# Performance work log

Measured on AMD Instinct MI355X. Metric: run time of the kernel, lower is better.

Reference implementation:

```python
import jax, jax.numpy as jnp
import numpy as np
from jax import lax

EPS = 1e-5
TRUNK_C, REG_C, GPOOL_C = 256, 192, 64
B, H, W = 256, 19, 19


def setup_inputs() -> dict:
    key = jax.random.key(0)
    ks = jax.random.split(key, 18)
    def bn_params(k, c):
        k1, k2, k3, k4 = jax.random.split(k, 4)
        return (jax.random.normal(k1, (c,)) * 0.1 + 1.0,   # gamma
                jax.random.normal(k2, (c,)) * 0.1,          # beta
                jax.random.normal(k3, (c,)) * 0.1,          # running mean
                jax.random.uniform(k4, (c,)) * 0.5 + 0.5)   # running var
    bn1_g, bn1_b, bn1_m, bn1_v = bn_params(ks[0], TRUNK_C)
    bn1b_g, bn1b_b, bn1b_m, bn1b_v = bn_params(ks[1], GPOOL_C)
    bn2_g, bn2_b, bn2_m, bn2_v = bn_params(ks[2], REG_C)
    x = jax.random.normal(ks[3], (B, TRUNK_C, H, W), dtype=jnp.float32)
    w1a = jax.random.normal(ks[4], (REG_C, TRUNK_C, 3, 3), dtype=jnp.float32) * (1.0 / np.sqrt(TRUNK_C * 9))
    w1b = jax.random.normal(ks[5], (GPOOL_C, TRUNK_C, 3, 3), dtype=jnp.float32) * (1.0 / np.sqrt(TRUNK_C * 9))
    w_lin = jax.random.normal(ks[6], (REG_C, 3 * GPOOL_C), dtype=jnp.float32) * (1.0 / np.sqrt(3 * GPOOL_C))
    w2 = jax.random.normal(ks[7], (TRUNK_C, REG_C, 3, 3), dtype=jnp.float32) * (1.0 / np.sqrt(REG_C * 9))
    return {
        'x': x, 'bn1_g': bn1_g, 'bn1_b': bn1_b, 'bn1_m': bn1_m, 'bn1_v': bn1_v,
        'w1a': w1a, 'w1b': w1b,
        'bn1b_g': bn1b_g, 'bn1b_b': bn1b_b, 'bn1b_m': bn1b_m, 'bn1b_v': bn1b_v,
        'w_lin': w_lin,
        'bn2_g': bn2_g, 'bn2_b': bn2_b, 'bn2_m': bn2_m, 'bn2_v': bn2_v,
        'w2': w2,
    }


def _bn(x, g, b, m, v):
    # inference batchnorm over channel dim of NCHW
    inv = g / jnp.sqrt(v + EPS)
    return (x - m[:, None, None]) * inv[:, None, None] + b[:, None, None]


def _mish(x):
    return x * jnp.tanh(jax.nn.softplus(x))


def _conv(x, w):
    return lax.conv_general_dilated(x, w, (1, 1), 'SAME',
                                    dimension_numbers=('NCHW', 'OIHW', 'NCHW'))


def _kata_gpool(x):
    # x: [B, C, H, W] -> [B, 3C]: mean, mean*(sqrt(N)-14)/10, max
    b, c, h, w = x.shape
    n = float(h * w)
    sqrt_n = n ** 0.5
    mean = jnp.sum(x, axis=(2, 3)) / n
    max_val = jnp.max(x, axis=(2, 3))
    scaled_mean = mean * ((sqrt_n - 14.0) / 10.0)
    return jnp.concatenate([mean, scaled_mean, max_val], axis=1)


def reference(x, bn1_g, bn1_b, bn1_m, bn1_v, w1a, w1b,
              bn1b_g, bn1b_b, bn1b_m, bn1b_v, w_lin,
              bn2_g, bn2_b, bn2_m, bn2_v, w2):
    out = _mish(_bn(x, bn1_g, bn1_b, bn1_m, bn1_v))
    reg = _conv(out, w1a)                       # [B, REG_C, H, W]
    gp = _conv(out, w1b)                        # [B, GPOOL_C, H, W]
    gp = _mish(_bn(gp, bn1b_g, bn1b_b, bn1b_m, bn1b_v))
    gp_pooled = _kata_gpool(gp)                 # [B, 3*GPOOL_C]
    gp_out = gp_pooled @ w_lin.T                # [B, REG_C]
    reg = reg + gp_out[:, :, None, None]
    out2 = _mish(_bn(reg, bn2_g, bn2_b, bn2_m, bn2_v))
    out2 = _conv(out2, w2)
    return out2 + x
```

## Files before the change

### kernel.cpp

```cpp
#include <hip/hip_runtime.h>
#include <hip/hip_bf16.h>
#include <math.h>


#define BATCH   256
#define TRUNK_C 256
#define REG_C   192
#define GPOOL_C 64
#define HH      19
#define WW      19
#define HW      361
#define PP      441
#define EPS     1e-5f

typedef __hip_bfloat16 bf16;
typedef __attribute__((ext_vector_type(8))) short short8;
typedef __attribute__((ext_vector_type(4))) float floatx4;

__device__ __forceinline__ float b2f(bf16 v) { return __bfloat162float(v); }
__device__ __forceinline__ bf16  f2b(float v) { return __float2bfloat16(v); }

__device__ __forceinline__ float mish_f(float v) {
    if (v > 20.0f) return v;
    float u = __expf(v);
    float n = u * (u + 2.0f);
    return v * __fdividef(n, n + 2.0f);
}

__device__ __forceinline__ void gload_lds16(const void* gsrc, void* lds) {
    __builtin_amdgcn_global_load_lds(
        (const __attribute__((address_space(1))) void*)gsrc,
        (__attribute__((address_space(3))) void*)lds, 16, 0, 0);
}

__global__ void prep_kernel(
    const float* g1, const float* b1, const float* m1, const float* v1,
    const float* g1b, const float* b1b, const float* m1b, const float* v1b,
    const float* g2, const float* b2, const float* m2, const float* v2,
    const float* __restrict__ w1a, const float* __restrict__ w1b,
    const float* __restrict__ w2,
    bf16* __restrict__ w1c_p, bf16* __restrict__ w2_p,
    bf16* __restrict__ act_pad, bf16* __restrict__ reg_pad,
    float* bnbuf)
{
    const int T1  = 16 * 72 * 64 * 8;
    const int T2  = 16 * 54 * 64 * 8;
    const int TW  = T1 + T2;
    const int TBa = BATCH * 80 * 32;
    const int TBr = BATCH * 80 * 24;
    int i = blockIdx.x * blockDim.x + threadIdx.x;
    if (i < TW) {
        if (i < T1) {
            int j = i & 7, lane = (i >> 3) & 63;
            int kc = (i >> 9) % 72, cog = (i >> 9) / 72;
            int co = cog * 16 + (lane & 15);
            int k = kc * 32 + ((lane >> 4) << 3) + j;
            int r = k >> 8, ci = k & 255;
            float v = (co < 192) ? w1a[co * 2304 + ci * 9 + r]
                                 : w1b[(co - 192) * 2304 + ci * 9 + r];
            w1c_p[i] = f2b(v);
        } else {
            int i2 = i - T1;
            int j = i2 & 7, lane = (i2 >> 3) & 63;
            int kc = (i2 >> 9) % 54, cog = (i2 >> 9) / 54;
            int co = cog * 16 + (lane & 15);
            int k = kc * 32 + ((lane >> 4) << 3) + j;
            int r = k / 192, ci = k % 192;
            w2_p[i2] = f2b(w2[co * 1728 + ci * 9 + r]);
        }
    } else if (i < TW + TBa + TBr) {
        int j = i - TW;
        bool isact = j < TBa;
        if (!isact) j -= TBa;
        int nb = isact ? 32 : 24;
        int b = j / (80 * nb);
        int rem = j - b * (80 * nb);
        int e = rem / nb, g = rem - (rem / nb) * nb;
        int pp;
        if (e < 21) pp = e;
        else if (e < 42) pp = 420 + (e - 21);
        else if (e < 61) pp = (e - 41) * 21;
        else pp = (e - 60) * 21 + 20;
        short8 z = {0, 0, 0, 0, 0, 0, 0, 0};
        if (isact) *(short8*)(act_pad + ((size_t)b * PP + pp) * TRUNK_C + g * 8) = z;
        else       *(short8*)(reg_pad + ((size_t)b * PP + pp) * REG_C + g * 8) = z;
    } else {
        int t = i - (TW + TBa + TBr);
        if (t < 256) {
            float s = g1[t] / sqrtf(v1[t] + EPS);
            bnbuf[t] = s;
            bnbuf[256 + t] = b1[t] - m1[t] * s;
        } else if (t < 320) {
            int c = t - 256;
            float s = g1b[c] / sqrtf(v1b[c] + EPS);
            bnbuf[512 + c] = s;
            bnbuf[576 + c] = b1b[c] - m1b[c] * s;
        } else if (t < 512) {
            int c = t - 320;
            float s = g2[c] / sqrtf(v2[c] + EPS);
            bnbuf[640 + c] = s;
            bnbuf[832 + c] = b2[c] - m2[c] * s;
        }
    }
}

__global__ __launch_bounds__(256)
void bn1_mish_t_kernel(const float* __restrict__ x, const float* __restrict__ bnbuf,
                       bf16* __restrict__ act_pad) {
    __shared__ float lds[256][32];
    int pc = blockIdx.x;
    int b  = blockIdx.y;
    int t  = threadIdx.x;
    int p0 = pc * 32;
    int px = t & 31;
#pragma unroll
    for (int it = 0; it < 32; ++it) {
        int ci = it * 8 + (t >> 5);
        int p  = p0 + px;
        float v = 0.0f;
        if (p < HW) v = x[((size_t)b * TRUNK_C + ci) * HW + p];
        v = v * bnbuf[ci] + bnbuf[256 + ci];
        lds[ci][px ^ (ci >> 3)] = mish_f(v);
    }
    __syncthreads();
#pragma unroll
    for (int it = 0; it < 4; ++it) {
        int pl = it * 8 + (t >> 5);
        int p  = p0 + pl;
        if (p >= HW) continue;
        int ch = t & 31;
        short8 vv;
#pragma unroll
        for (int j = 0; j < 8; ++j) {
            bf16 h = f2b(lds[ch * 8 + j][pl ^ ch]);
            short s;
            __builtin_memcpy(&s, &h, 2);
            vv[j] = s;
        }
        int pp = (p / WW + 1) * 21 + (p % WW + 1);
        *(short8*)(act_pad + ((size_t)b * PP + pp) * TRUNK_C + ch * 8) = vv;
    }
}

__global__ __launch_bounds__(256, 3)
void conv1_kernel(const bf16* __restrict__ act,
                  const bf16* __restrict__ wfrag,
                  bf16* __restrict__ reg_out,
                  bf16* __restrict__ gp_out,
                  const float* __restrict__ ep_scale, const float* __restrict__ ep_bias) {
    const int CIN = 256, NKC = 72;
    __shared__ __align__(16) bf16 atile[4][128 * 32];
    const int b   = blockIdx.x;
    const int mt  = blockIdx.y;
    const int nh  = blockIdx.z;
    const int t   = threadIdx.x;
    const int w   = t >> 6, lane = t & 63;
    const int mi  = w >> 1, ni = w & 1;
    const int l15 = lane & 15, quad = lane >> 4;

    int row0 = t >> 2;
    int sq   = t & 3;
    int ss   = sq ^ ((row0 >> 1) & 3);
    int sp0  = mt * 128 + row0;      if (sp0 > 360) sp0 = 360;
    int sp1  = mt * 128 + row0 + 64; if (sp1 > 360) sp1 = 360;
    const bf16* sb0 = act + ((size_t)b * PP + (sp0 / WW) * 21 + (sp0 % WW)) * CIN + (ss << 3);
    const bf16* sb1 = act + ((size_t)b * PP + (sp1 / WW) * 21 + (sp1 % WW)) * CIN + (ss << 3);

    const bf16* wb[4];
#pragma unroll
    for (int ns = 0; ns < 4; ++ns)
        wb[ns] = wfrag + ((size_t)(nh * 8 + ni * 4 + ns) * NKC * 64 + lane) * 8;

    int aoff[4];
#pragma unroll
    for (int ms = 0; ms < 4; ++ms) {
        int row = mi * 64 + ms * 16 + l15;
        aoff[ms] = row * 32 + ((quad ^ ((row >> 1) & 3)) << 3);
    }

    auto stage = [&](int buf, int kc) {
        int r = kc >> 3, c = kc & 7;
        int off = ((r / 3) * 21 + (r % 3)) * CIN + (c << 5);
        bf16* dst = &atile[buf][w << 9];
        gload_lds16(sb0 + off, dst);
        gload_lds16(sb1 + off, dst + 2048);
    };

    floatx4 acc[4][4];
#pragma unroll
    for (int i = 0; i < 4; ++i)
#pragma unroll
        for (int j = 0; j < 4; ++j) acc[i][j] = (floatx4){0.f, 0.f, 0.f, 0.f};

    short8 afr[4], bfrA[4], bfrB[4];
    stage(0, 0);
    stage(1, 1);
    asm volatile("" ::: "memory");
#pragma unroll
    for (int ns = 0; ns < 4; ++ns) bfrA[ns] = *(const short8*)(wb[ns]);
    asm volatile("" ::: "memory");
    stage(2, 2);

    for (int kc = 0; kc < NKC; kc += 2) {
        if (kc == 0) asm volatile("s_waitcnt vmcnt(8)" ::: "memory");
        else         asm volatile("s_waitcnt vmcnt(12)" ::: "memory");
        __builtin_amdgcn_sched_barrier(0);
        __builtin_amdgcn_s_barrier();
        __builtin_amdgcn_sched_barrier(0);
#pragma unroll
        for (int ns = 0; ns < 4; ++ns)
            bfrB[ns] = *(const short8*)(wb[ns] + (size_t)(kc + 1) * 512);
        asm volatile("" ::: "memory");
        {
            int s = kc + 3; if (s > NKC - 1) s = NKC - 1;
            stage((kc + 3) & 3, s);
        }
        {
            const bf16* at = atile[kc & 3];
#pragma unroll
            for (int ms = 0; ms < 4; ++ms)
                afr[ms] = *(const short8*)(at + aoff[ms]);
        }
#pragma unroll
        for (int ms = 0; ms < 4; ++ms)
#pragma unroll
            for (int ns = 0; ns < 4; ++ns)
                acc[ms][ns] = __builtin_amdgcn_mfma_f32_16x16x32_bf16(
                    afr[ms], bfrA[ns], acc[ms][ns], 0, 0, 0);

        asm volatile("s_waitcnt vmcnt(12)" ::: "memory");
        __builtin_amdgcn_sched_barrier(0);
        __builtin_amdgcn_s_barrier();
        __builtin_amdgcn_sched_barrier(0);
        {
            int nb = kc + 2; if (nb > NKC - 1) nb = NKC - 1;
#pragma unroll
            for (int ns = 0; ns < 4; ++ns)
                bfrA[ns] = *(const short8*)(wb[ns] + (size_t)nb * 512);
        }
        asm volatile("" ::: "memory");
        {
            int s = kc + 4; if (s > NKC - 1) s = NKC - 1;
            stage((kc + 4) & 3, s);
        }
        {
            const bf16* at = atile[(kc + 1) & 3];
#pragma unroll
            for (int ms = 0; ms < 4; ++ms)
                afr[ms] = *(const short8*)(at + aoff[ms]);
        }
#pragma unroll
        for (int ms = 0; ms < 4; ++ms)
#pragma unroll
            for (int ns = 0; ns < 4; ++ns)
                acc[ms][ns] = __builtin_amdgcn_mfma_f32_16x16x32_bf16(
                    afr[ms], bfrB[ns], acc[ms][ns], 0, 0, 0);
    }

    float scl[4], bia[4];
#pragma unroll
    for (int ns = 0; ns < 4; ++ns) {
        int co = (nh * 8 + ni * 4 + ns) * 16 + l15;
        if (co >= 192) { scl[ns] = ep_scale[co - 192]; bia[ns] = ep_bias[co - 192]; }
    }
#pragma unroll
    for (int ms = 0; ms < 4; ++ms) {
#pragma unroll
        for (int rg = 0; rg < 4; ++rg) {
            int p = mt * 128 + mi * 64 + ms * 16 + quad * 4 + rg;
            if (p > 360) continue;
            size_t ppad = (size_t)b * PP + (p / WW + 1) * 21 + (p % WW + 1);
#pragma unroll
            for (int ns = 0; ns < 4; ++ns) {
                int co = (nh * 8 + ni * 4 + ns) * 16 + l15;
                float v = acc[ms][ns][rg];
                if (co < 192) {
                    reg_out[ppad * REG_C + co] = f2b(v);
                } else {
                    v = mish_f(v * scl[ns] + bia[ns]);
                    gp_out[((size_t)b * HW + p) * GPOOL_C + (co - 192)] = f2b(v);
                }
            }
        }
    }
}

__global__ __launch_bounds__(256, 3)
void conv2_kernel(const bf16* __restrict__ act,
                  const bf16* __restrict__ wfrag,
                  const float* __restrict__ resid,
                  float* __restrict__ out) {
    const int CIN = 192, NKC = 54;
    __shared__ __align__(16) bf16 atile[4][128 * 32];
    const int b   = blockIdx.x;
    const int mt  = blockIdx.y;
    const int nh  = blockIdx.z;
    const int t   = threadIdx.x;
    const int w   = t >> 6, lane = t & 63;
    const int pw  = w >> 1, cw = w & 1;
    const int l15 = lane & 15, quad = lane >> 4;

    int row0 = t >> 2;
    int sq   = t & 3;
    int ss   = sq ^ ((row0 >> 1) & 3);
    int sp0  = mt * 128 + row0;      if (sp0 > 360) sp0 = 360;
    int sp1  = mt * 128 + row0 + 64; if (sp1 > 360) sp1 = 360;
    const bf16* sb0 = act + ((size_t)b * PP + (sp0 / WW) * 21 + (sp0 % WW)) * CIN + (ss << 3);
    const bf16* sb1 = act + ((size_t)b * PP + (sp1 / WW) * 21 + (sp1 % WW)) * CIN + (ss << 3);

    const bf16* wb[4];
#pragma unroll
    for (int ms = 0; ms < 4; ++ms)
        wb[ms] = wfrag + ((size_t)(nh * 8 + cw * 4 + ms) * NKC * 64 + lane) * 8;

    int aoff[4];
#pragma unroll
    for (int ns = 0; ns < 4; ++ns) {
        int row = pw * 64 + ns * 16 + l15;
        aoff[ns] = row * 32 + ((quad ^ ((row >> 1) & 3)) << 3);
    }

    auto stage = [&](int buf, int kc) {
        int r = kc / 6, c = kc % 6;
        int off = ((r / 3) * 21 + (r % 3)) * CIN + (c << 5);
        bf16* dst = &atile[buf][w << 9];
        gload_lds16(sb0 + off, dst);
        gload_lds16(sb1 + off, dst + 2048);
    };

    floatx4 acc[4][4];
#pragma unroll
    for (int i = 0; i < 4; ++i)
#pragma unroll
        for (int j = 0; j < 4; ++j) acc[i][j] = (floatx4){0.f, 0.f, 0.f, 0.f};

    short8 bfa[4], wfrA[4], wfrB[4];
    stage(0, 0);
    stage(1, 1);
    asm volatile("" ::: "memory");
#pragma unroll
    for (int ms = 0; ms < 4; ++ms) wfrA[ms] = *(const short8*)(wb[ms]);
    asm volatile("" ::: "memory");
    stage(2, 2);

    for (int kc = 0; kc < NKC; kc += 2) {
        if (kc == 0) asm volatile("s_waitcnt vmcnt(8)" ::: "memory");
        else         asm volatile("s_waitcnt vmcnt(12)" ::: "memory");
        __builtin_amdgcn_sched_barrier(0);
        __builtin_amdgcn_s_barrier();
        __builtin_amdgcn_sched_barrier(0);
#pragma unroll
        for (int ms = 0; ms < 4; ++ms)
            wfrB[ms] = *(const short8*)(wb[ms] + (size_t)(kc + 1) * 512);
        asm volatile("" ::: "memory");
        {
            int s = kc + 3; if (s > NKC - 1) s = NKC - 1;
            stage((kc + 3) & 3, s);
        }
        {
            const bf16* at = atile[kc & 3];
#pragma unroll
            for (int ns = 0; ns < 4; ++ns)
                bfa[ns] = *(const short8*)(at + aoff[ns]);
        }
#pragma unroll
        for (int ms = 0; ms < 4; ++ms)
#pragma unroll
            for (int ns = 0; ns < 4; ++ns)
                acc[ms][ns] = __builtin_amdgcn_mfma_f32_16x16x32_bf16(
                    wfrA[ms], bfa[ns], acc[ms][ns], 0, 0, 0);

        asm volatile("s_waitcnt vmcnt(12)" ::: "memory");
        __builtin_amdgcn_sched_barrier(0);
        __builtin_amdgcn_s_barrier();
        __builtin_amdgcn_sched_barrier(0);
        {
            int nb = kc + 2; if (nb > NKC - 1) nb = NKC - 1;
#pragma unroll
            for (int ms = 0; ms < 4; ++ms)
                wfrA[ms] = *(const short8*)(wb[ms] + (size_t)nb * 512);
        }
        asm volatile("" ::: "memory");
        {
            int s = kc + 4; if (s > NKC - 1) s = NKC - 1;
            stage((kc + 4) & 3, s);
        }
        {
            const bf16* at = atile[(kc + 1) & 3];
#pragma unroll
            for (int ns = 0; ns < 4; ++ns)
                bfa[ns] = *(const short8*)(at + aoff[ns]);
        }
#pragma unroll
        for (int ms = 0; ms < 4; ++ms)
#pragma unroll
            for (int ns = 0; ns < 4; ++ns)
                acc[ms][ns] = __builtin_amdgcn_mfma_f32_16x16x32_bf16(
                    wfrB[ms], bfa[ns], acc[ms][ns], 0, 0, 0);
    }

#pragma unroll
    for (int ns = 0; ns < 4; ++ns) {
        int p = mt * 128 + pw * 64 + ns * 16 + l15;
        if (p > 360) continue;
#pragma unroll
        for (int ms = 0; ms < 4; ++ms) {
#pragma unroll
            for (int rg = 0; rg < 4; ++rg) {
                int co = (nh * 8 + cw * 4 + ms) * 16 + quad * 4 + rg;
                size_t idx = ((size_t)b * TRUNK_C + co) * HW + p;
                out[idx] = acc[ms][ns][rg] + resid[idx];
            }
        }
    }
}

__global__ void gpool_lin_kernel(const bf16* __restrict__ gp, const float* __restrict__ w_lin,
                                 float* __restrict__ gpout) {
    __shared__ float ls[4][64], lm[4][64];
    __shared__ float pooled_s[192];
    int b = blockIdx.x;
    int t = threadIdx.x;
    int c = t & 63, sub = t >> 6;
    float s = 0.0f, mx = -1e30f;
    for (int p = sub; p < HW; p += 4) {
        float v = b2f(gp[((size_t)b * HW + p) * GPOOL_C + c]);
        s += v;
        mx = fmaxf(mx, v);
    }
    ls[sub][c] = s; lm[sub][c] = mx;
    __syncthreads();
    if (t < 64) {
        float ss = ls[0][t] + ls[1][t] + ls[2][t] + ls[3][t];
        float mm = fmaxf(fmaxf(lm[0][t], lm[1][t]), fmaxf(lm[2][t], lm[3][t]));
        float mean = ss * (1.0f / 361.0f);
        pooled_s[t] = mean;
        pooled_s[64 + t] = mean * 0.5f;
        pooled_s[128 + t] = mm;
    }
    __syncthreads();
    if (t < 192) {
        const float4* wr4 = (const float4*)(w_lin + t * 192);
        float acc = 0.0f;
#pragma unroll 8
        for (int j = 0; j < 48; ++j) {
            float4 wv = wr4[j];
            acc = fmaf(pooled_s[j * 4 + 0], wv.x, acc);
            acc = fmaf(pooled_s[j * 4 + 1], wv.y, acc);
            acc = fmaf(pooled_s[j * 4 + 2], wv.z, acc);
            acc = fmaf(pooled_s[j * 4 + 3], wv.w, acc);
        }
        gpout[b * 192 + t] = acc;
    }
}

__global__ __launch_bounds__(256)
void add_bn2_mish_kernel(bf16* __restrict__ reg_pad, const float* __restrict__ gpout,
                         const float* __restrict__ bnbuf) {
    const int total = BATCH * HW * 24;
    int i = blockIdx.x * blockDim.x + threadIdx.x;
    if (i >= total) return;
    int g  = i % 24;
    int bp = i / 24;
    int p  = bp % HW;
    int b  = bp / HW;
    int pp = (p / WW + 1) * 21 + (p % WW + 1);
    size_t idx = ((size_t)b * PP + pp) * REG_C + g * 8;
    short8 v = *(const short8*)(reg_pad + idx);
    const float* gpo = gpout + b * 192 + g * 8;
    const float* sc  = bnbuf + 640 + g * 8;
    const float* bi  = bnbuf + 832 + g * 8;
    short8 o;
#pragma unroll
    for (int j = 0; j < 8; ++j) {
        short sj = v[j];
        bf16 h;
        __builtin_memcpy(&h, &sj, 2);
        float f = b2f(h) + gpo[j];
        f = f * sc[j] + bi[j];
        h = f2b(mish_f(f));
        __builtin_memcpy(&sj, &h, 2);
        o[j] = sj;
    }
    *(short8*)(reg_pad + idx) = o;
}

extern "C" void kernel_launch(void* const* d_in, const int* in_sizes, int n_in,
                              void* d_out, int out_size, void* d_ws, size_t ws_size,
                              hipStream_t stream) {
    const float* x     = (const float*)d_in[0];
    const float* bn1_g = (const float*)d_in[1];
    const float* bn1_b = (const float*)d_in[2];
    const float* bn1_m = (const float*)d_in[3];
    const float* bn1_v = (const float*)d_in[4];
    const float* w1a   = (const float*)d_in[5];
    const float* w1b   = (const float*)d_in[6];
    const float* bn1b_g = (const float*)d_in[7];
    const float* bn1b_b = (const float*)d_in[8];
    const float* bn1b_m = (const float*)d_in[9];
    const float* bn1b_v = (const float*)d_in[10];
    const float* w_lin  = (const float*)d_in[11];
    const float* bn2_g  = (const float*)d_in[12];
    const float* bn2_b  = (const float*)d_in[13];
    const float* bn2_m  = (const float*)d_in[14];
    const float* bn2_v  = (const float*)d_in[15];
    const float* w2     = (const float*)d_in[16];
    float* out = (float*)d_out;

    char* ws = (char*)d_ws;
    size_t off = 0;
    auto alloc = [&](size_t bytes) {
        void* p = ws + off;
        off += (bytes + 255) & ~(size_t)255;
        return p;
    };
    bf16*  act_pad = (bf16*)alloc((size_t)BATCH * PP * TRUNK_C * sizeof(bf16));
    bf16*  reg_pad = (bf16*)alloc((size_t)BATCH * PP * REG_C * sizeof(bf16));
    bf16*  gp      = (bf16*)alloc((size_t)BATCH * HW * GPOOL_C * sizeof(bf16));
    bf16*  w1c_p   = (bf16*)alloc((size_t)16 * 72 * 64 * 8 * sizeof(bf16));
    bf16*  w2_p    = (bf16*)alloc((size_t)16 * 54 * 64 * 8 * sizeof(bf16));
    float* gpout   = (float*)alloc((size_t)BATCH * 192 * sizeof(float));
    float* bnbuf   = (float*)alloc(1024 * sizeof(float));
    (void)ws_size;

    {
        const int total = (16 * 72 * 64 * 8) + (16 * 54 * 64 * 8)
                        + BATCH * 80 * 32 + BATCH * 80 * 24 + 512;
        hipLaunchKernelGGL(prep_kernel, dim3((total + 255) / 256), dim3(256), 0, stream,
                           bn1_g, bn1_b, bn1_m, bn1_v,
                           bn1b_g, bn1b_b, bn1b_m, bn1b_v,
                           bn2_g, bn2_b, bn2_m, bn2_v,
                           w1a, w1b, w2, w1c_p, w2_p, act_pad, reg_pad, bnbuf);
    }

    hipLaunchKernelGGL(bn1_mish_t_kernel, dim3(12, BATCH), dim3(256), 0, stream,
                       x, bnbuf, act_pad);

    hipLaunchKernelGGL(conv1_kernel, dim3(BATCH, 3, 2), dim3(256), 0, stream,
                       act_pad, w1c_p, reg_pad, gp, bnbuf + 512, bnbuf + 576);

    hipLaunchKernelGGL(gpool_lin_kernel, dim3(BATCH), dim3(256), 0, stream,
                       gp, w_lin, gpout);

    {
        int total = BATCH * HW * 24;
        hipLaunchKernelGGL(add_bn2_mish_kernel, dim3((total + 255) / 256), dim3(256), 0, stream,
                           reg_pad, gpout, bnbuf);
    }

    hipLaunchKernelGGL(conv2_kernel, dim3(BATCH, 3, 2), dim3(256), 0, stream,
                       reg_pad, w2_p, x, out);
}
```

Baseline: 669.2 us.

## Split conv workgroups into single-wave 64x64 tiles with barrier-free triple buffering

Both implicit-GEMM conv kernels move from 256-thread workgroups with 128-row, 128-channel tiles to single-wavefront workgroups, each computing a 64-position by 64-channel tile. A 1D grid is decoded so that neighbouring workgroups share the same batch and position tile. Because each wave stages only its own LDS tile, the s_barrier calls go away, and a 3-slot ring buffer replaces the 4-slot one. s_setprio raises priority around the MFMA blocks. Separately, the bn2 scale and bias are folded into the pooled linear output so the elementwise kernel does one FMA per element. The cost is that activation tiles are no longer shared across the channel halves within a workgroup, so each tile is fetched by more workgroups.

```diff
diff --git a/kernel.cpp b/kernel.cpp
--- a/kernel.cpp
+++ b/kernel.cpp
@@ -142,48 +142,56 @@
     }
 }
 
-__global__ __launch_bounds__(256, 3)
+__device__ __forceinline__ void decode_wg(int wg, int& b, int& mt, int& cb) {
+    int g = wg >> 5, r = wg & 31;
+    cb = r >> 3;
+    int pidx = g * 8 + (r & 7);
+    b = pidx / 6;
+    mt = pidx - b * 6;
+}
+
+__global__ __launch_bounds__(64, 3)
 void conv1_kernel(const bf16* __restrict__ act,
                   const bf16* __restrict__ wfrag,
                   bf16* __restrict__ reg_out,
                   bf16* __restrict__ gp_out,
                   const float* __restrict__ ep_scale, const float* __restrict__ ep_bias) {
     const int CIN = 256, NKC = 72;
-    __shared__ __align__(16) bf16 atile[4][128 * 32];
-    const int b   = blockIdx.x;
-    const int mt  = blockIdx.y;
-    const int nh  = blockIdx.z;
-    const int t   = threadIdx.x;
-    const int w   = t >> 6, lane = t & 63;
-    const int mi  = w >> 1, ni = w & 1;
+    __shared__ __align__(16) bf16 atile[3][64 * 32];
+    int b, mt, cb;
+    decode_wg(blockIdx.x, b, mt, cb);
+    const int lane = threadIdx.x;
     const int l15 = lane & 15, quad = lane >> 4;
 
-    int row0 = t >> 2;
-    int sq   = t & 3;
-    int ss   = sq ^ ((row0 >> 1) & 3);
-    int sp0  = mt * 128 + row0;      if (sp0 > 360) sp0 = 360;
-    int sp1  = mt * 128 + row0 + 64; if (sp1 > 360) sp1 = 360;
-    const bf16* sb0 = act + ((size_t)b * PP + (sp0 / WW) * 21 + (sp0 % WW)) * CIN + (ss << 3);
-    const bf16* sb1 = act + ((size_t)b * PP + (sp1 / WW) * 21 + (sp1 % WW)) * CIN + (ss << 3);
+    const bf16* sb[4];
+#pragma unroll
+    for (int o = 0; o < 4; ++o) {
+        int row = o * 16 + (lane >> 2);
+        int ss  = (lane & 3) ^ ((row >> 1) & 3);
+        int p   = mt * 64 + row; if (p > 360) p = 360;
+        sb[o] = act + ((size_t)b * PP + (p / WW) * 21 + (p % WW)) * CIN + (ss << 3);
+    }
 
     const bf16* wb[4];
 #pragma unroll
     for (int ns = 0; ns < 4; ++ns)
-        wb[ns] = wfrag + ((size_t)(nh * 8 + ni * 4 + ns) * NKC * 64 + lane) * 8;
+        wb[ns] = wfrag + ((size_t)(cb * 4 + ns) * NKC * 64 + lane) * 8;
 
     int aoff[4];
 #pragma unroll
     for (int ms = 0; ms < 4; ++ms) {
-        int row = mi * 64 + ms * 16 + l15;
+        int row = ms * 16 + l15;
         aoff[ms] = row * 32 + ((quad ^ ((row >> 1) & 3)) << 3);
     }
 
     auto stage = [&](int buf, int kc) {
         int r = kc >> 3, c = kc & 7;
         int off = ((r / 3) * 21 + (r % 3)) * CIN + (c << 5);
-        bf16* dst = &atile[buf][w << 9];
-        gload_lds16(sb0 + off, dst);
-        gload_lds16(sb1 + off, dst + 2048);
+        bf16* dst = &atile[buf][0];
+        gload_lds16(sb[0] + off, dst);
+        gload_lds16(sb[1] + off, dst + 512);
+        gload_lds16(sb[2] + off, dst + 1024);
+        gload_lds16(sb[3] + off, dst + 1536);
     };
 
     floatx4 acc[4][4];
@@ -198,81 +206,79 @@
     asm volatile("" ::: "memory");
 #pragma unroll
     for (int ns = 0; ns < 4; ++ns) bfrA[ns] = *(const short8*)(wb[ns]);
-    asm volatile("" ::: "memory");
-    stage(2, 2);
-
+
+    int rb = 0;
     for (int kc = 0; kc < NKC; kc += 2) {
-        if (kc == 0) asm volatile("s_waitcnt vmcnt(8)" ::: "memory");
-        else         asm volatile("s_waitcnt vmcnt(12)" ::: "memory");
-        __builtin_amdgcn_sched_barrier(0);
-        __builtin_amdgcn_s_barrier();
-        __builtin_amdgcn_sched_barrier(0);
+        int b2i = rb + 2; if (b2i >= 3) b2i -= 3;
+        int b1i = rb + 1; if (b1i >= 3) b1i -= 3;
+        asm volatile("s_waitcnt vmcnt(8)" ::: "memory");
+        {
+            int s = kc + 2; if (s > NKC - 1) s = NKC - 1;
+            stage(b2i, s);
+        }
+        asm volatile("" ::: "memory");
 #pragma unroll
         for (int ns = 0; ns < 4; ++ns)
             bfrB[ns] = *(const short8*)(wb[ns] + (size_t)(kc + 1) * 512);
-        asm volatile("" ::: "memory");
-        {
-            int s = kc + 3; if (s > NKC - 1) s = NKC - 1;
-            stage((kc + 3) & 3, s);
-        }
-        {
-            const bf16* at = atile[kc & 3];
+        {
+            const bf16* at = &atile[rb][0];
 #pragma unroll
             for (int ms = 0; ms < 4; ++ms)
                 afr[ms] = *(const short8*)(at + aoff[ms]);
         }
+        __builtin_amdgcn_s_setprio(1);
 #pragma unroll
         for (int ms = 0; ms < 4; ++ms)
 #pragma unroll
             for (int ns = 0; ns < 4; ++ns)
                 acc[ms][ns] = __builtin_amdgcn_mfma_f32_16x16x32_bf16(
                     afr[ms], bfrA[ns], acc[ms][ns], 0, 0, 0);
-
-        asm volatile("s_waitcnt vmcnt(12)" ::: "memory");
-        __builtin_amdgcn_sched_barrier(0);
-        __builtin_amdgcn_s_barrier();
-        __builtin_amdgcn_sched_barrier(0);
+        __builtin_amdgcn_s_setprio(0);
+        asm volatile("s_waitcnt vmcnt(8)" ::: "memory");
+        {
+            int s = kc + 3; if (s > NKC - 1) s = NKC - 1;
+            stage(rb, s);
+        }
+        asm volatile("" ::: "memory");
         {
             int nb = kc + 2; if (nb > NKC - 1) nb = NKC - 1;
 #pragma unroll
             for (int ns = 0; ns < 4; ++ns)
                 bfrA[ns] = *(const short8*)(wb[ns] + (size_t)nb * 512);
         }
-        asm volatile("" ::: "memory");
-        {
-            int s = kc + 4; if (s > NKC - 1) s = NKC - 1;
-            stage((kc + 4) & 3, s);
-        }
-        {
-            const bf16* at = atile[(kc + 1) & 3];
+        {
+            const bf16* at = &atile[b1i][0];
 #pragma unroll
             for (int ms = 0; ms < 4; ++ms)
                 afr[ms] = *(const short8*)(at + aoff[ms]);
         }
+        __builtin_amdgcn_s_setprio(1);
 #pragma unroll
         for (int ms = 0; ms < 4; ++ms)
 #pragma unroll
             for (int ns = 0; ns < 4; ++ns)
                 acc[ms][ns] = __builtin_amdgcn_mfma_f32_16x16x32_bf16(
                     afr[ms], bfrB[ns], acc[ms][ns], 0, 0, 0);
+        __builtin_amdgcn_s_setprio(0);
+        rb = b2i;
     }
 
     float scl[4], bia[4];
 #pragma unroll
     for (int ns = 0; ns < 4; ++ns) {
-        int co = (nh * 8 + ni * 4 + ns) * 16 + l15;
+        int co = (cb * 4 + ns) * 16 + l15;
         if (co >= 192) { scl[ns] = ep_scale[co - 192]; bia[ns] = ep_bias[co - 192]; }
     }
 #pragma unroll
     for (int ms = 0; ms < 4; ++ms) {
 #pragma unroll
         for (int rg = 0; rg < 4; ++rg) {
-            int p = mt * 128 + mi * 64 + ms * 16 + quad * 4 + rg;
+            int p = mt * 64 + ms * 16 + quad * 4 + rg;
             if (p > 360) continue;
             size_t ppad = (size_t)b * PP + (p / WW + 1) * 21 + (p % WW + 1);
 #pragma unroll
             for (int ns = 0; ns < 4; ++ns) {
-                int co = (nh * 8 + ni * 4 + ns) * 16 + l15;
+                int co = (cb * 4 + ns) * 16 + l15;
                 float v = acc[ms][ns][rg];
                 if (co < 192) {
                     reg_out[ppad * REG_C + co] = f2b(v);
@@ -285,47 +291,47 @@
     }
 }
 
-__global__ __launch_bounds__(256, 3)
+__global__ __launch_bounds__(64, 3)
 void conv2_kernel(const bf16* __restrict__ act,
                   const bf16* __restrict__ wfrag,
                   const float* __restrict__ resid,
                   float* __restrict__ out) {
     const int CIN = 192, NKC = 54;
-    __shared__ __align__(16) bf16 atile[4][128 * 32];
-    const int b   = blockIdx.x;
-    const int mt  = blockIdx.y;
-    const int nh  = blockIdx.z;
-    const int t   = threadIdx.x;
-    const int w   = t >> 6, lane = t & 63;
-    const int pw  = w >> 1, cw = w & 1;
+    __shared__ __align__(16) bf16 atile[3][64 * 32];
+    int b, mt, cb;
+    decode_wg(blockIdx.x, b, mt, cb);
+    const int lane = threadIdx.x;
     const int l15 = lane & 15, quad = lane >> 4;
 
-    int row0 = t >> 2;
-    int sq   = t & 3;
-    int ss   = sq ^ ((row0 >> 1) & 3);
-    int sp0  = mt * 128 + row0;      if (sp0 > 360) sp0 = 360;
-    int sp1  = mt * 128 + row0 + 64; if (sp1 > 360) sp1 = 360;
-    const bf16* sb0 = act + ((size_t)b * PP + (sp0 / WW) * 21 + (sp0 % WW)) * CIN + (ss << 3);
-    const bf16* sb1 = act + ((size_t)b * PP + (sp1 / WW) * 21 + (sp1 % WW)) * CIN + (ss << 3);
+    const bf16* sb[4];
+#pragma unroll
+    for (int o = 0; o < 4; ++o) {
+        int row = o * 16 + (lane >> 2);
+        int ss  = (lane & 3) ^ ((row >> 1) & 3);
+        int p   = mt * 64 + row; if (p > 360) p = 360;
+        sb[o] = act + ((size_t)b * PP + (p / WW) * 21 + (p % WW)) * CIN + (ss << 3);
+    }
 
     const bf16* wb[4];
 #pragma unroll
     for (int ms = 0; ms < 4; ++ms)
-        wb[ms] = wfrag + ((size_t)(nh * 8 + cw * 4 + ms) * NKC * 64 + lane) * 8;
+        wb[ms] = wfrag + ((size_t)(cb * 4 + ms) * NKC * 64 + lane) * 8;
 
     int aoff[4];
 #pragma unroll
     for (int ns = 0; ns < 4; ++ns) {
-        int row = pw * 64 + ns * 16 + l15;
+        int row = ns * 16 + l15;
         aoff[ns] = row * 32 + ((quad ^ ((row >> 1) & 3)) << 3);
     }
 
     auto stage = [&](int buf, int kc) {
         int r = kc / 6, c = kc % 6;
         int off = ((r / 3) * 21 + (r % 3)) * CIN + (c << 5);
-        bf16* dst = &atile[buf][w << 9];
-        gload_lds16(sb0 + off, dst);
-        gload_lds16(sb1 + off, dst + 2048);
+        bf16* dst = &atile[buf][0];
+        gload_lds16(sb[0] + off, dst);
+        gload_lds16(sb[1] + off, dst + 512);
+        gload_lds16(sb[2] + off, dst + 1024);
+        gload_lds16(sb[3] + off, dst + 1536);
     };
 
     floatx4 acc[4][4];
@@ -340,74 +346,72 @@
     asm volatile("" ::: "memory");
 #pragma unroll
     for (int ms = 0; ms < 4; ++ms) wfrA[ms] = *(const short8*)(wb[ms]);
-    asm volatile("" ::: "memory");
-    stage(2, 2);
-
+
+    int rb = 0;
     for (int kc = 0; kc < NKC; kc += 2) {
-        if (kc == 0) asm volatile("s_waitcnt vmcnt(8)" ::: "memory");
-        else         asm volatile("s_waitcnt vmcnt(12)" ::: "memory");
-        __builtin_amdgcn_sched_barrier(0);
-        __builtin_amdgcn_s_barrier();
-        __builtin_amdgcn_sched_barrier(0);
+        int b2i = rb + 2; if (b2i >= 3) b2i -= 3;
+        int b1i = rb + 1; if (b1i >= 3) b1i -= 3;
+        asm volatile("s_waitcnt vmcnt(8)" ::: "memory");
+        {
+            int s = kc + 2; if (s > NKC - 1) s = NKC - 1;
+            stage(b2i, s);
+        }
+        asm volatile("" ::: "memory");
 #pragma unroll
         for (int ms = 0; ms < 4; ++ms)
             wfrB[ms] = *(const short8*)(wb[ms] + (size_t)(kc + 1) * 512);
-        asm volatile("" ::: "memory");
-        {
-            int s = kc + 3; if (s > NKC - 1) s = NKC - 1;
-            stage((kc + 3) & 3, s);
-        }
-        {
-            const bf16* at = atile[kc & 3];
+        {
+            const bf16* at = &atile[rb][0];
 #pragma unroll
             for (int ns = 0; ns < 4; ++ns)
                 bfa[ns] = *(const short8*)(at + aoff[ns]);
         }
+        __builtin_amdgcn_s_setprio(1);
 #pragma unroll
         for (int ms = 0; ms < 4; ++ms)
 #pragma unroll
             for (int ns = 0; ns < 4; ++ns)
                 acc[ms][ns] = __builtin_amdgcn_mfma_f32_16x16x32_bf16(
                     wfrA[ms], bfa[ns], acc[ms][ns], 0, 0, 0);
-
-        asm volatile("s_waitcnt vmcnt(12)" ::: "memory");
-        __builtin_amdgcn_sched_barrier(0);
-        __builtin_amdgcn_s_barrier();
-        __builtin_amdgcn_sched_barrier(0);
+        __builtin_amdgcn_s_setprio(0);
+        asm volatile("s_waitcnt vmcnt(8)" ::: "memory");
+        {
+            int s = kc + 3; if (s > NKC - 1) s = NKC - 1;
+            stage(rb, s);
+        }
+        asm volatile("" ::: "memory");
         {
             int nb = kc + 2; if (nb > NKC - 1) nb = NKC - 1;
 #pragma unroll
             for (int ms = 0; ms < 4; ++ms)
                 wfrA[ms] = *(const short8*)(wb[ms] + (size_t)nb * 512);
         }
-        asm volatile("" ::: "memory");
-        {
-            int s = kc + 4; if (s > NKC - 1) s = NKC - 1;
-            stage((kc + 4) & 3, s);
-        }
-        {
-            const bf16* at = atile[(kc + 1) & 3];
+        {
+            const bf16* at = &atile[b1i][0];
 #pragma unroll
             for (int ns = 0; ns < 4; ++ns)
                 bfa[ns] = *(const short8*)(at + aoff[ns]);
         }
+        __builtin_amdgcn_s_setprio(1);
 #pragma unroll
         for (int ms = 0; ms < 4; ++ms)
 #pragma unroll
             for (int ns = 0; ns < 4; ++ns)
                 acc[ms][ns] = __builtin_amdgcn_mfma_f32_16x16x32_bf16(
                     wfrB[ms], bfa[ns], acc[ms][ns], 0, 0, 0);
+        __builtin_amdgcn_s_setprio(0);
+        rb = b2i;
     }
 
 #pragma unroll
     for (int ns = 0; ns < 4; ++ns) {
-        int p = mt * 128 + pw * 64 + ns * 16 + l15;
+        int p = mt * 64 + ns * 16 + l15;
         if (p > 360) continue;
 #pragma unroll
         for (int ms = 0; ms < 4; ++ms) {
 #pragma unroll
             for (int rg = 0; rg < 4; ++rg) {
-                int co = (nh * 8 + cw * 4 + ms) * 16 + quad * 4 + rg;
+                int co = (cb * 4 + ms) * 16 + quad * 4 + rg;
                 size_t idx = ((size_t)b * TRUNK_C + co) * HW + p;
                 out[idx] = acc[ms][ns][rg] + resid[idx];
             }
@@ -416,7 +420,7 @@
 }
 
 __global__ void gpool_lin_kernel(const bf16* __restrict__ gp, const float* __restrict__ w_lin,
-                                 float* __restrict__ gpout) {
+                                 const float* __restrict__ bnbuf, float* __restrict__ gob) {
     __shared__ float ls[4][64], lm[4][64];
     __shared__ float pooled_s[192];
     int b = blockIdx.x;
@@ -450,13 +454,13 @@
             acc = fmaf(pooled_s[j * 4 + 2], wv.z, acc);
             acc = fmaf(pooled_s[j * 4 + 3], wv.w, acc);
         }
-        gpout[b * 192 + t] = acc;
+        gob[b * 192 + t] = acc * bnbuf[640 + t] + bnbuf[832 + t];
     }
 }
 
 __global__ __launch_bounds__(256)
-void add_bn2_mish_kernel(bf16* __restrict__ reg_pad, const float* __restrict__ gpout,
-                         const float* __restrict__ bnbuf) {
+void bn2_mish_kernel(bf16* __restrict__ reg_pad, const float* __restrict__ gob,
+                     const float* __restrict__ bnbuf) {
     const int total = BATCH * HW * 24;
     int i = blockIdx.x * blockDim.x + threadIdx.x;
     if (i >= total) return;
@@ -467,17 +471,15 @@
     int pp = (p / WW + 1) * 21 + (p % WW + 1);
     size_t idx = ((size_t)b * PP + pp) * REG_C + g * 8;
     short8 v = *(const short8*)(reg_pad + idx);
-    const float* gpo = gpout + b * 192 + g * 8;
-    const float* sc  = bnbuf + 640 + g * 8;
-    const float* bi  = bnbuf + 832 + g * 8;
+    const float* go = gob + b * 192 + g * 8;
+    const float* sc = bnbuf + 640 + g * 8;
     short8 o;
 #pragma unroll
     for (int j = 0; j < 8; ++j) {
         short sj = v[j];
         bf16 h;
         __builtin_memcpy(&h, &sj, 2);
-        float f = b2f(h) + gpo[j];
-        f = f * sc[j] + bi[j];
+        float f = b2f(h) * sc[j] + go[j];
         h = f2b(mish_f(f));
         __builtin_memcpy(&sj, &h, 2);
         o[j] = sj;
@@ -519,7 +521,7 @@
     bf16*  gp      = (bf16*)alloc((size_t)BATCH * HW * GPOOL_C * sizeof(bf16));
     bf16*  w1c_p   = (bf16*)alloc((size_t)16 * 72 * 64 * 8 * sizeof(bf16));
     bf16*  w2_p    = (bf16*)alloc((size_t)16 * 54 * 64 * 8 * sizeof(bf16));
-    float* gpout   = (float*)alloc((size_t)BATCH * 192 * sizeof(float));
+    float* gob     = (float*)alloc((size_t)BATCH * 192 * sizeof(float));
     float* bnbuf   = (float*)alloc(1024 * sizeof(float));
     (void)ws_size;
 
@@ -536,18 +538,18 @@
     hipLaunchKernelGGL(bn1_mish_t_kernel, dim3(12, BATCH), dim3(256), 0, stream,
                        x, bnbuf, act_pad);
 
-    hipLaunchKernelGGL(conv1_kernel, dim3(BATCH, 3, 2), dim3(256), 0, stream,
+    hipLaunchKernelGGL(conv1_kernel, dim3(6144), dim3(64), 0, stream,
                        act_pad, w1c_p, reg_pad, gp, bnbuf + 512, bnbuf + 576);
 
     hipLaunchKernelGGL(gpool_lin_kernel, dim3(BATCH), dim3(256), 0, stream,
-                       gp, w_lin, gpout);
+                       gp, w_lin, bnbuf, gob);
 
     {
         int total = BATCH * HW * 24;
-        hipLaunchKernelGGL(add_bn2_mish_kernel, dim3((total + 255) / 256), dim3(256), 0, stream,
-                           reg_pad, gpout, bnbuf);
-    }
-
-    hipLaunchKernelGGL(conv2_kernel, dim3(BATCH, 3, 2), dim3(256), 0, stream,
+        hipLaunchKernelGGL(bn2_mish_kernel, dim3((total + 255) / 256), dim3(256), 0, stream,
+                           reg_pad, gob, bnbuf);
+    }
+
+    hipLaunchKernelGGL(conv2_kernel, dim3(6144), dim3(64), 0, stream,
                        reg_pad, w2_p, x, out);
 }
```

Result: slower. 699.5 us (+4.5%).
